# Optimization experiments

Measured on AMD Instinct MI355X. Metric: run time of the kernel, lower is better.

The kernel has to match this reference:

```python
import jax, jax.numpy as jnp
import numpy as np

B, S, HID = 2, 2048, 4096
NH, NKV, D = 32, 8, 128
GROUPS = NH // NKV


def _rotate_half(x):
    x1, x2 = jnp.split(x, 2, axis=-1)
    return jnp.concatenate((-x2, x1), axis=-1)


def setup_inputs() -> dict:
    key = jax.random.key(0)
    ks = jax.random.split(key, 5)
    hidden_states = jax.random.normal(ks[0], (B, S, HID), jnp.float32)
    Wq = jax.random.normal(ks[1], (HID, NH * D), jnp.float32) * (1.0 / np.float32(np.sqrt(HID)))
    Wk = jax.random.normal(ks[2], (HID, NKV * D), jnp.float32) * (1.0 / np.float32(np.sqrt(HID)))
    Wv = jax.random.normal(ks[3], (HID, NKV * D), jnp.float32) * (1.0 / np.float32(np.sqrt(HID)))
    Wo = jax.random.normal(ks[4], (NH * D, HID), jnp.float32) * (1.0 / np.float32(np.sqrt(NH * D)))
    # RoPE caches (Llama-style, base 10000)
    inv_freq = (1.0 / (10000.0 ** (np.arange(0, D, 2, dtype=np.float32) / D))).astype(np.float32)
    t = np.arange(S, dtype=np.float32)
    freqs = np.outer(t, inv_freq)  # [S, D/2]
    emb = np.concatenate([freqs, freqs], axis=-1)  # [S, D]
    cos_cache = jnp.asarray(np.cos(emb), jnp.float32)
    sin_cache = jnp.asarray(np.sin(emb), jnp.float32)
    position_ids = jnp.broadcast_to(jnp.arange(S, dtype=jnp.int64), (B, S))
    # causal mask used by scaled_qk's torch.where (True = attend)
    causal = jnp.tril(jnp.ones((S, S), dtype=bool))
    attention_mask = jnp.broadcast_to(causal[None, None], (B, 1, S, S))
    return {
        "hidden_states": hidden_states, "Wq": Wq, "Wk": Wk, "Wv": Wv, "Wo": Wo,
        "cos_cache": cos_cache, "sin_cache": sin_cache,
        "position_ids": position_ids, "attention_mask": attention_mask,
    }


def reference(hidden_states, Wq, Wk, Wv, Wo, cos_cache, sin_cache, position_ids, attention_mask):
    b, s, _ = hidden_states.shape
    # qkv_proj + move_heads_front -> [b, heads, s, d]
    Q = (hidden_states @ Wq).reshape(b, s, NH, D).transpose(0, 2, 1, 3)
    K = (hidden_states @ Wk).reshape(b, s, NKV, D).transpose(0, 2, 1, 3)
    V = (hidden_states @ Wv).reshape(b, s, NKV, D).transpose(0, 2, 1, 3)
    # RoPE
    cos = cos_cache[position_ids][:, None]  # [b,1,s,d]
    sin = sin_cache[position_ids][:, None]
    Q = Q * cos + _rotate_half(Q) * sin
    K = K * cos + _rotate_half(K) * sin
    # repeat_kv
    K = jnp.repeat(K, GROUPS, axis=1)  # [b,NH,s,d]
    V = jnp.repeat(V, GROUPS, axis=1)
    # scaled QK + mask + softmax (fp32) + PV
    scores = jnp.einsum("bhsd,bhtd->bhst", Q, K) / np.float32(np.sqrt(D))
    scores = jnp.where(attention_mask, scores, jnp.finfo(scores.dtype).min)
    probs = jax.nn.softmax(scores.astype(jnp.float32), axis=-1).astype(Q.dtype)
    attn = jnp.einsum("bhst,bhtd->bhsd", probs, V)
    # o_proj
    out = attn.transpose(0, 2, 1, 3).reshape(b, s, NH * D) @ Wo
    return out
```

## Files before the change

### kernel.cpp

```cpp
#include <hip/hip_runtime.h>

#define B_ 2
#define S_ 2048
#define HID_ 4096
#define NH_ 32
#define NKV_ 8
#define D_ 128
#define M_ (B_*S_)
#define NQKV_ (HID_ + 2*NKV_*D_)

typedef __bf16 v8bf __attribute__((ext_vector_type(8)));
typedef float  v4f  __attribute__((ext_vector_type(4)));

__device__ __forceinline__ unsigned short f2bf(float x) {
    unsigned u = __float_as_uint(x);
    u += 0x7FFFu + ((u >> 16) & 1u);
    return (unsigned short)(u >> 16);
}
__device__ __forceinline__ float bf2f(unsigned short h) {
    return __uint_as_float(((unsigned)h) << 16);
}

__device__ __forceinline__ void gl_lds16(const unsigned short* g, unsigned short* l) {
    __builtin_amdgcn_global_load_lds(
        (const __attribute__((address_space(1))) void*)g,
        (__attribute__((address_space(3))) void*)l, 16, 0, 0);
}

__global__ __launch_bounds__(256)
void cvt_f32_bf16(const float* __restrict__ src, unsigned short* __restrict__ dst, int n4) {
    int i = blockIdx.x * 256 + threadIdx.x;
    if (i >= n4) return;
    float4 v = ((const float4*)src)[i];
    ushort4 o;
    o.x = f2bf(v.x); o.y = f2bf(v.y); o.z = f2bf(v.z); o.w = f2bf(v.w);
    ((ushort4*)dst)[i] = o;
}

__global__ __launch_bounds__(256)
void transpose_f32_bf16(const float* __restrict__ src,
                        unsigned short* __restrict__ dst, int K, int N) {
    __shared__ unsigned short tile[64][65];
    int n0 = blockIdx.x * 64, k0 = blockIdx.y * 64;
    int tid = threadIdx.x;
    for (int i = 0; i < 16; ++i) {
        int fi = tid + i * 256;
        int r = fi >> 6, c = fi & 63;
        tile[r][c] = f2bf(src[(size_t)(k0 + r) * N + n0 + c]);
    }
    __syncthreads();
    for (int i = 0; i < 16; ++i) {
        int fi = tid + i * 256;
        int r = fi >> 6, c = fi & 63;
        dst[(size_t)(n0 + r) * K + k0 + c] = tile[c][r];
    }
}

__global__ __launch_bounds__(256)
void transpose_v(const unsigned short* __restrict__ src,
                 unsigned short* __restrict__ dst) {
    __shared__ unsigned short tile[64][65];
    int s0 = blockIdx.x * 64, d0 = blockIdx.y * 64;
    size_t base = (size_t)blockIdx.z * S_ * D_;
    int tid = threadIdx.x;
    for (int i = 0; i < 16; ++i) {
        int fi = tid + i * 256;
        int r = fi >> 6, c = fi & 63;
        tile[r][c] = src[base + (size_t)(s0 + r) * D_ + d0 + c];
    }
    __syncthreads();
    for (int i = 0; i < 16; ++i) {
        int fi = tid + i * 256;
        int r = fi >> 6, c = fi & 63;
        dst[base + (size_t)(d0 + r) * S_ + s0 + c] = tile[c][r];
    }
}

template <int MODE>
__global__ __launch_bounds__(256)
void gemm_bt(const unsigned short* __restrict__ A,
             const unsigned short* __restrict__ BT,
             int K, int lda, int ldb,
             unsigned short* __restrict__ outQ,
             unsigned short* __restrict__ outK,
             unsigned short* __restrict__ outV,
             float* __restrict__ outF) {
    __shared__ unsigned short As[128][32];
    __shared__ unsigned short Bs[128][32];
    int tid = threadIdx.x;
    int lane = tid & 63, wid = tid >> 6;
    int quad = lane >> 4, l16 = lane & 15;
    int wr = wid >> 1, wc = wid & 1;
    int r0 = blockIdx.y * 128, n0 = blockIdx.x * 128;

    v4f zero = {0.f, 0.f, 0.f, 0.f};
    v4f acc[4][4];
    for (int i = 0; i < 4; ++i) for (int j = 0; j < 4; ++j) acc[i][j] = zero;

    const int srow = wid * 32 + (lane >> 2);
    const int sch  = (lane & 3) * 8;
    const unsigned short* gA = &A [(size_t)(r0 + srow) * lda + sch];
    const unsigned short* gB = &BT[(size_t)(n0 + srow) * ldb + sch];
    unsigned short* lA0 = &As[wid * 32][0];
    unsigned short* lA1 = &As[wid * 32 + 16][0];
    unsigned short* lB0 = &Bs[wid * 32][0];
    unsigned short* lB1 = &Bs[wid * 32 + 16][0];

    for (int kt = 0; kt < K / 32; ++kt) {
        int kk = kt * 32;
        gl_lds16(gA + kk, lA0);
        gl_lds16(gA + (size_t)16 * lda + kk, lA1);
        gl_lds16(gB + kk, lB0);
        gl_lds16(gB + (size_t)16 * ldb + kk, lB1);
        __syncthreads();
        v8bf av[4], bv[4];
        for (int ms = 0; ms < 4; ++ms) av[ms] = *(const v8bf*)&As[wr * 64 + ms * 16 + l16][quad * 8];
        for (int ns = 0; ns < 4; ++ns) bv[ns] = *(const v8bf*)&Bs[wc * 64 + ns * 16 + l16][quad * 8];
        for (int ms = 0; ms < 4; ++ms)
            for (int ns = 0; ns < 4; ++ns)
                acc[ms][ns] = __builtin_amdgcn_mfma_f32_16x16x32_bf16(av[ms], bv[ns], acc[ms][ns], 0, 0, 0);
        __syncthreads();
    }

    for (int ms = 0; ms < 4; ++ms)
        for (int ns = 0; ns < 4; ++ns)
            for (int r = 0; r < 4; ++r) {
                int row = r0 + wr * 64 + ms * 16 + quad * 4 + r;
                int col = n0 + wc * 64 + ns * 16 + l16;
                if (MODE == 1) {
                    outF[(size_t)row * HID_ + col] = acc[ms][ns][r];
                } else {
                    unsigned short hv = f2bf(acc[ms][ns][r]);
                    int b = row >> 11, s = row & (S_ - 1);
                    if (col < HID_) {
                        int h = col >> 7, d = col & 127;
                        outQ[((size_t)((b * NH_ + h) * S_ + s)) * D_ + d] = hv;
                    } else if (col < HID_ + NKV_ * D_) {
                        int j = col - HID_; int h = j >> 7, d = j & 127;
                        outK[((size_t)((b * NKV_ + h) * S_ + s)) * D_ + d] = hv;
                    } else {
                        int j = col - HID_ - NKV_ * D_; int h = j >> 7, d = j & 127;
                        outV[((size_t)((b * NKV_ + h) * S_ + s)) * D_ + d] = hv;
                    }
                }
            }
}

__global__ __launch_bounds__(256)
void rope_kernel(unsigned short* __restrict__ buf,
                 const float* __restrict__ cosc,
                 const float* __restrict__ sinc, int total) {
    int idx = blockIdx.x * 256 + threadIdx.x;
    if (idx >= total) return;
    int d2 = idx & 63;
    int s  = (idx >> 6) & (S_ - 1);
    int bh = idx >> 17;
    size_t base = ((size_t)bh * S_ + s) * D_;
    float c  = cosc[s * D_ + d2];
    float sn = sinc[s * D_ + d2];
    float x1 = bf2f(buf[base + d2]);
    float x2 = bf2f(buf[base + d2 + 64]);
    buf[base + d2]      = f2bf(x1 * c - x2 * sn);
    buf[base + d2 + 64] = f2bf(x2 * c + x1 * sn);
}

__global__ __launch_bounds__(256)
void flash_attn(const unsigned short* __restrict__ Q,
                const unsigned short* __restrict__ Kb,
                const unsigned short* __restrict__ VT,
                unsigned short* __restrict__ O) {
    __shared__ unsigned short Ks[64][136];
    __shared__ unsigned short Vt[128][72];
    __shared__ unsigned short Ps[4][16][72];
    int tid = threadIdx.x;
    int lane = tid & 63, w = tid >> 6;
    int quad = lane >> 4, l16 = lane & 15;
    int qt = blockIdx.x, h = blockIdx.y, b = blockIdx.z;
    int qbase = qt * 64 + w * 16;

    const size_t qoff = ((size_t)(b * NH_ + h) * S_ + qbase + l16) * D_;
    v8bf aq[4];
    for (int kt = 0; kt < 4; ++kt) aq[kt] = *(const v8bf*)&Q[qoff + kt * 32 + quad * 8];

    const int hkv = h >> 2;
    const size_t kvbase = (size_t)(b * NKV_ + hkv) * S_ * D_;
    const size_t vtbase = kvbase;

    int krow[4], kch[4], vrow[4], vch[4];
    for (int i = 0; i < 4; ++i) {
        int idx = tid + i * 256;
        krow[i] = idx >> 4; kch[i] = idx & 15;
        vrow[i] = idx >> 3; vch[i] = idx & 7;
    }

    v4f zero = {0.f, 0.f, 0.f, 0.f};
    v4f o[8];
    for (int i = 0; i < 8; ++i) o[i] = zero;
    float m_[4] = {-1e30f, -1e30f, -1e30f, -1e30f};
    float l_[4] = {0.f, 0.f, 0.f, 0.f};

    const int ntiles = qt + 1;
    uint4 kpre[4], vpre[4];
    for (int i = 0; i < 4; ++i) {
        kpre[i] = *(const uint4*)&Kb[kvbase + (size_t)krow[i] * D_ + kch[i] * 8];
        vpre[i] = *(const uint4*)&VT[vtbase + (size_t)vrow[i] * S_ + vch[i] * 8];
    }

    for (int t = 0; t < ntiles; ++t) {
        int kv0 = t * 64;
        __syncthreads();
        for (int i = 0; i < 4; ++i) {
            *(uint4*)&Ks[krow[i]][kch[i] * 8] = kpre[i];
            *(uint4*)&Vt[vrow[i]][vch[i] * 8] = vpre[i];
        }
        __syncthreads();
        if (t + 1 < ntiles) {
            int nkv0 = kv0 + 64;
            for (int i = 0; i < 4; ++i) {
                kpre[i] = *(const uint4*)&Kb[kvbase + (size_t)(nkv0 + krow[i]) * D_ + kch[i] * 8];
                vpre[i] = *(const uint4*)&VT[vtbase + (size_t)vrow[i] * S_ + nkv0 + vch[i] * 8];
            }
        }

        v4f sa[4];
        for (int kg = 0; kg < 4; ++kg) sa[kg] = zero;
        for (int kg = 0; kg < 4; ++kg)
            for (int kt = 0; kt < 4; ++kt) {
                v8bf bk = *(const v8bf*)&Ks[kg * 16 + l16][kt * 32 + quad * 8];
                sa[kg] = __builtin_amdgcn_mfma_f32_16x16x32_bf16(aq[kt], bk, sa[kg], 0, 0, 0);
            }

        const float scale = 0.08838834764831845f;
        const bool diag = (t == qt);
        float p[4][4], al[4];
        for (int r = 0; r < 4; ++r) {
            int qrow = qbase + quad * 4 + r;
            float s0 = sa[0][r] * scale, s1 = sa[1][r] * scale;
            float s2 = sa[2][r] * scale, s3 = sa[3][r] * scale;
            if (diag) {
                if (kv0      + l16 > qrow) s0 = -1e30f;
                if (kv0 + 16 + l16 > qrow) s1 = -1e30f;
                if (kv0 + 32 + l16 > qrow) s2 = -1e30f;
                if (kv0 + 48 + l16 > qrow) s3 = -1e30f;
            }
            float rm = fmaxf(fmaxf(s0, s1), fmaxf(s2, s3));
            rm = fmaxf(rm, __shfl_xor(rm, 1));
            rm = fmaxf(rm, __shfl_xor(rm, 2));
            rm = fmaxf(rm, __shfl_xor(rm, 4));
            rm = fmaxf(rm, __shfl_xor(rm, 8));
            float mn = fmaxf(m_[r], rm);
            al[r] = __expf(m_[r] - mn);
            float p0 = __expf(s0 - mn), p1 = __expf(s1 - mn);
            float p2 = __expf(s2 - mn), p3 = __expf(s3 - mn);
            p[0][r] = p0; p[1][r] = p1; p[2][r] = p2; p[3][r] = p3;
            float rs = (p0 + p1) + (p2 + p3);
            rs += __shfl_xor(rs, 1);
            rs += __shfl_xor(rs, 2);
            rs += __shfl_xor(rs, 4);
            rs += __shfl_xor(rs, 8);
            l_[r] = l_[r] * al[r] + rs;
            m_[r] = mn;
        }
        for (int i = 0; i < 8; ++i)
            for (int r = 0; r < 4; ++r) o[i][r] *= al[r];

        for (int kg = 0; kg < 4; ++kg)
            for (int r = 0; r < 4; ++r)
                Ps[w][quad * 4 + r][kg * 16 + l16] = f2bf(p[kg][r]);
        v8bf pa0 = *(const v8bf*)&Ps[w][l16][quad * 8];
        v8bf pa1 = *(const v8bf*)&Ps[w][l16][32 + quad * 8];
        for (int n8 = 0; n8 < 8; ++n8) {
            v8bf bv0 = *(const v8bf*)&Vt[n8 * 16 + l16][quad * 8];
            v8bf bv1 = *(const v8bf*)&Vt[n8 * 16 + l16][32 + quad * 8];
            o[n8] = __builtin_amdgcn_mfma_f32_16x16x32_bf16(pa0, bv0, o[n8], 0, 0, 0);
            o[n8] = __builtin_amdgcn_mfma_f32_16x16x32_bf16(pa1, bv1, o[n8], 0, 0, 0);
        }
    }

    for (int n8 = 0; n8 < 8; ++n8)
        for (int r = 0; r < 4; ++r) {
            int qg = qbase + quad * 4 + r;
            float val = o[n8][r] / l_[r];
            O[((size_t)(b * S_ + qg)) * HID_ + h * D_ + n8 * 16 + l16] = f2bf(val);
        }
}

extern "C" void kernel_launch(void* const* d_in, const int* in_sizes, int n_in,
                              void* d_out, int out_size, void* d_ws, size_t ws_size,
                              hipStream_t stream) {
    const float* hid  = (const float*)d_in[0];
    const float* Wq   = (const float*)d_in[1];
    const float* Wk   = (const float*)d_in[2];
    const float* Wv   = (const float*)d_in[3];
    const float* Wo   = (const float*)d_in[4];
    const float* cosc = (const float*)d_in[5];
    const float* sinc = (const float*)d_in[6];

    unsigned short* ws    = (unsigned short*)d_ws;
    unsigned short* wqkvT = ws;
    unsigned short* qbuf  = ws + (size_t)NQKV_ * HID_;
    unsigned short* kbuf  = qbuf + (size_t)B_ * NH_ * S_ * D_;
    unsigned short* vbuf  = kbuf + (size_t)B_ * NKV_ * S_ * D_;
    unsigned short* hidB  = vbuf + (size_t)B_ * NKV_ * S_ * D_;
    unsigned short* attn  = ws;
    unsigned short* woT   = ws + (size_t)M_ * HID_;
    unsigned short* vTbuf = hidB;

    cvt_f32_bf16<<<(M_ * HID_ / 4 + 255) / 256, 256, 0, stream>>>(hid, hidB, M_ * HID_ / 4);
    transpose_f32_bf16<<<dim3(64, 64), 256, 0, stream>>>(Wq, wqkvT, HID_, HID_);
    transpose_f32_bf16<<<dim3(16, 64), 256, 0, stream>>>(Wk, wqkvT + (size_t)HID_ * HID_, HID_, NKV_ * D_);
    transpose_f32_bf16<<<dim3(16, 64), 256, 0, stream>>>(Wv, wqkvT + (size_t)(HID_ + NKV_ * D_) * HID_, HID_, NKV_ * D_);
    gemm_bt<0><<<dim3(NQKV_ / 128, M_ / 128), 256, 0, stream>>>(
        hidB, wqkvT, HID_, HID_, HID_, qbuf, kbuf, vbuf, nullptr);
    rope_kernel<<<(B_ * NH_ * S_ * 64) / 256, 256, 0, stream>>>(qbuf, cosc, sinc, B_ * NH_ * S_ * 64);
    rope_kernel<<<(B_ * NKV_ * S_ * 64) / 256, 256, 0, stream>>>(kbuf, cosc, sinc, B_ * NKV_ * S_ * 64);
    transpose_v<<<dim3(S_ / 64, D_ / 64, B_ * NKV_), 256, 0, stream>>>(vbuf, vTbuf);
    flash_attn<<<dim3(S_ / 64, NH_, B_), 256, 0, stream>>>(qbuf, kbuf, vTbuf, attn);
    transpose_f32_bf16<<<dim3(64, 64), 256, 0, stream>>>(Wo, woT, HID_, HID_);
    gemm_bt<1><<<dim3(HID_ / 128, M_ / 128), 256, 0, stream>>>(
        attn, woT, HID_, HID_, HID_, nullptr, nullptr, nullptr, (float*)d_out);
}
```

Measured before the change: 1.318 ms.

## Rewrite flash attention with 32x32 MFMA, 128-row Q tiles and register-resident P

The flash attention kernel moves from 16x16x32 to 32x32x16 bf16 MFMA and computes S transposed, so each lane owns one query row; row max and sum then need only a single cross-half shuffle. P stays in registers and is exchanged through lane shuffles instead of an LDS round trip. Q tiles grow to 128 rows per block and are scheduled longest-first, K in LDS gets an XOR swizzle to avoid bank conflicts, and softmax uses exp2 with a folded scale. The larger Q tile raises register pressure and may lower occupancy, and waves whose rows are already finished idle on barriers during the last K tiles.

```diff
diff --git a/kernel.cpp b/kernel.cpp
--- a/kernel.cpp
+++ b/kernel.cpp
@@ -11,6 +11,7 @@
 
 typedef __bf16 v8bf __attribute__((ext_vector_type(8)));
 typedef float  v4f  __attribute__((ext_vector_type(4)));
+typedef float  v16f __attribute__((ext_vector_type(16)));
 
 __device__ __forceinline__ unsigned short f2bf(float x) {
     unsigned u = __float_as_uint(x);
@@ -19,6 +20,12 @@
 }
 __device__ __forceinline__ float bf2f(unsigned short h) {
     return __uint_as_float(((unsigned)h) << 16);
+}
+__device__ __forceinline__ unsigned pack2bf(float a, float b) {
+    return (unsigned)f2bf(a) | ((unsigned)f2bf(b) << 16);
+}
+__device__ __forceinline__ float exp2g(float x) {
+    return __builtin_amdgcn_exp2f(x);
 }
 
 __device__ __forceinline__ void gl_lds16(const unsigned short* g, unsigned short* l) {
@@ -169,119 +176,154 @@
                 const unsigned short* __restrict__ Kb,
                 const unsigned short* __restrict__ VT,
                 unsigned short* __restrict__ O) {
-    __shared__ unsigned short Ks[64][136];
+    __shared__ unsigned short Ks[64 * 128];
     __shared__ unsigned short Vt[128][72];
-    __shared__ unsigned short Ps[4][16][72];
     int tid = threadIdx.x;
     int lane = tid & 63, w = tid >> 6;
-    int quad = lane >> 4, l16 = lane & 15;
-    int qt = blockIdx.x, h = blockIdx.y, b = blockIdx.z;
-    int qbase = qt * 64 + w * 16;
-
-    const size_t qoff = ((size_t)(b * NH_ + h) * S_ + qbase + l16) * D_;
-    v8bf aq[4];
-    for (int kt = 0; kt < 4; ++kt) aq[kt] = *(const v8bf*)&Q[qoff + kt * 32 + quad * 8];
+    int l31 = lane & 31, hi = lane >> 5;
+    int qt = 15 - (int)blockIdx.x;
+    int h = blockIdx.y, b = blockIdx.z;
+    int qbase = qt * 128 + w * 32;
+
+    const size_t qoff = ((size_t)(b * NH_ + h) * S_ + qbase + l31) * D_ + hi * 8;
+    v8bf aq[8];
+    #pragma unroll
+    for (int kt = 0; kt < 8; ++kt) aq[kt] = *(const v8bf*)&Q[qoff + kt * 16];
 
     const int hkv = h >> 2;
     const size_t kvbase = (size_t)(b * NKV_ + hkv) * S_ * D_;
     const size_t vtbase = kvbase;
 
     int krow[4], kch[4], vrow[4], vch[4];
+    #pragma unroll
     for (int i = 0; i < 4; ++i) {
         int idx = tid + i * 256;
         krow[i] = idx >> 4; kch[i] = idx & 15;
         vrow[i] = idx >> 3; vch[i] = idx & 7;
     }
 
-    v4f zero = {0.f, 0.f, 0.f, 0.f};
-    v4f o[8];
-    for (int i = 0; i < 8; ++i) o[i] = zero;
-    float m_[4] = {-1e30f, -1e30f, -1e30f, -1e30f};
-    float l_[4] = {0.f, 0.f, 0.f, 0.f};
-
-    const int ntiles = qt + 1;
+    v16f o[4];
+    #pragma unroll
+    for (int n = 0; n < 4; ++n)
+        #pragma unroll
+        for (int r = 0; r < 16; ++r) o[n][r] = 0.f;
+    float m2 = -1e30f, l_ = 0.f;
+
+    const int ntB = 2 * qt + 2;
+    const int twmax = (qbase + 31) >> 6;
+
     uint4 kpre[4], vpre[4];
+    #pragma unroll
     for (int i = 0; i < 4; ++i) {
         kpre[i] = *(const uint4*)&Kb[kvbase + (size_t)krow[i] * D_ + kch[i] * 8];
         vpre[i] = *(const uint4*)&VT[vtbase + (size_t)vrow[i] * S_ + vch[i] * 8];
     }
 
-    for (int t = 0; t < ntiles; ++t) {
+    for (int t = 0; t < ntB; ++t) {
         int kv0 = t * 64;
         __syncthreads();
+        #pragma unroll
         for (int i = 0; i < 4; ++i) {
-            *(uint4*)&Ks[krow[i]][kch[i] * 8] = kpre[i];
+            *(uint4*)&Ks[(size_t)krow[i] * 128 + ((kch[i] * 8) ^ ((krow[i] & 7) << 3))] = kpre[i];
             *(uint4*)&Vt[vrow[i]][vch[i] * 8] = vpre[i];
         }
         __syncthreads();
-        if (t + 1 < ntiles) {
+        if (t + 1 < ntB) {
             int nkv0 = kv0 + 64;
+            #pragma unroll
             for (int i = 0; i < 4; ++i) {
                 kpre[i] = *(const uint4*)&Kb[kvbase + (size_t)(nkv0 + krow[i]) * D_ + kch[i] * 8];
                 vpre[i] = *(const uint4*)&VT[vtbase + (size_t)vrow[i] * S_ + nkv0 + vch[i] * 8];
             }
         }
-
-        v4f sa[4];
-        for (int kg = 0; kg < 4; ++kg) sa[kg] = zero;
-        for (int kg = 0; kg < 4; ++kg)
-            for (int kt = 0; kt < 4; ++kt) {
-                v8bf bk = *(const v8bf*)&Ks[kg * 16 + l16][kt * 32 + quad * 8];
-                sa[kg] = __builtin_amdgcn_mfma_f32_16x16x32_bf16(aq[kt], bk, sa[kg], 0, 0, 0);
+        if (t > twmax) continue;
+
+        v16f s0, s1;
+        #pragma unroll
+        for (int r = 0; r < 16; ++r) { s0[r] = 0.f; s1[r] = 0.f; }
+        #pragma unroll
+        for (int kt = 0; kt < 8; ++kt) {
+            int cw = (kt * 16 + hi * 8) ^ ((l31 & 7) << 3);
+            v8bf k0 = *(const v8bf*)&Ks[(size_t)l31 * 128 + cw];
+            v8bf k1 = *(const v8bf*)&Ks[(size_t)(32 + l31) * 128 + cw];
+            s0 = __builtin_amdgcn_mfma_f32_32x32x16_bf16(k0, aq[kt], s0, 0, 0, 0);
+            s1 = __builtin_amdgcn_mfma_f32_32x32x16_bf16(k1, aq[kt], s1, 0, 0, 0);
+        }
+
+        if (kv0 + 63 > qbase) {
+            int vq = qbase + l31 - kv0 - 4 * hi;
+            #pragma unroll
+            for (int r = 0; r < 16; ++r) {
+                int c0 = (r & 3) + 8 * (r >> 2);
+                if (c0 > vq)      s0[r] = -1e30f;
+                if (c0 + 32 > vq) s1[r] = -1e30f;
             }
-
-        const float scale = 0.08838834764831845f;
-        const bool diag = (t == qt);
-        float p[4][4], al[4];
-        for (int r = 0; r < 4; ++r) {
-            int qrow = qbase + quad * 4 + r;
-            float s0 = sa[0][r] * scale, s1 = sa[1][r] * scale;
-            float s2 = sa[2][r] * scale, s3 = sa[3][r] * scale;
-            if (diag) {
-                if (kv0      + l16 > qrow) s0 = -1e30f;
-                if (kv0 + 16 + l16 > qrow) s1 = -1e30f;
-                if (kv0 + 32 + l16 > qrow) s2 = -1e30f;
-                if (kv0 + 48 + l16 > qrow) s3 = -1e30f;
+        }
+        float rm = fmaxf(s0[0], s1[0]);
+        #pragma unroll
+        for (int r = 1; r < 16; ++r) rm = fmaxf(rm, fmaxf(s0[r], s1[r]));
+        rm = fmaxf(rm, __shfl_xor(rm, 32));
+        const float cexp = 0.1275279431f;
+        float m2n = fmaxf(m2, rm * cexp);
+        float al = exp2g(m2 - m2n);
+        float rs = 0.f;
+        #pragma unroll
+        for (int r = 0; r < 16; ++r) {
+            s0[r] = exp2g(__builtin_fmaf(s0[r], cexp, -m2n));
+            s1[r] = exp2g(__builtin_fmaf(s1[r], cexp, -m2n));
+            rs += s0[r] + s1[r];
+        }
+        rs += __shfl_xor(rs, 32);
+        l_ = l_ * al + rs;
+        m2 = m2n;
+        #pragma unroll
+        for (int n = 0; n < 4; ++n)
+            #pragma unroll
+            for (int r = 0; r < 16; ++r) o[n][r] *= al;
+
+        unsigned pk0[4][2], pk1[4][2];
+        #pragma unroll
+        for (int g = 0; g < 4; ++g) {
+            pk0[g][0] = pack2bf(s0[4*g],   s0[4*g+1]);
+            pk0[g][1] = pack2bf(s0[4*g+2], s0[4*g+3]);
+            pk1[g][0] = pack2bf(s1[4*g],   s1[4*g+1]);
+            pk1[g][1] = pack2bf(s1[4*g+2], s1[4*g+3]);
+        }
+        const bool hb = (hi != 0);
+        #pragma unroll
+        for (int kb = 0; kb < 4; ++kb) {
+            const int g0 = (kb & 1) * 2;
+            unsigned la, lb, oa, ob;
+            if (kb < 2) { la = pk0[g0][0]; lb = pk0[g0][1]; oa = pk0[g0+1][0]; ob = pk0[g0+1][1]; }
+            else        { la = pk1[g0][0]; lb = pk1[g0][1]; oa = pk1[g0+1][0]; ob = pk1[g0+1][1]; }
+            unsigned sa0 = hb ? la : oa, sa1 = hb ? lb : ob;
+            unsigned ra0 = (unsigned)__shfl_xor((int)sa0, 32);
+            unsigned ra1 = (unsigned)__shfl_xor((int)sa1, 32);
+            unsigned ma0 = hb ? oa : la, ma1 = hb ? ob : lb;
+            union { unsigned u[4]; v8bf v; } pf;
+            pf.u[0] = hb ? ra0 : ma0; pf.u[1] = hb ? ra1 : ma1;
+            pf.u[2] = hb ? ma0 : ra0; pf.u[3] = hb ? ma1 : ra1;
+            #pragma unroll
+            for (int n = 0; n < 4; ++n) {
+                v8bf av = *(const v8bf*)&Vt[n * 32 + l31][kb * 16 + hi * 8];
+                o[n] = __builtin_amdgcn_mfma_f32_32x32x16_bf16(av, pf.v, o[n], 0, 0, 0);
             }
-            float rm = fmaxf(fmaxf(s0, s1), fmaxf(s2, s3));
-            rm = fmaxf(rm, __shfl_xor(rm, 1));
-            rm = fmaxf(rm, __shfl_xor(rm, 2));
-            rm = fmaxf(rm, __shfl_xor(rm, 4));
-            rm = fmaxf(rm, __shfl_xor(rm, 8));
-            float mn = fmaxf(m_[r], rm);
-            al[r] = __expf(m_[r] - mn);
-            float p0 = __expf(s0 - mn), p1 = __expf(s1 - mn);
-            float p2 = __expf(s2 - mn), p3 = __expf(s3 - mn);
-            p[0][r] = p0; p[1][r] = p1; p[2][r] = p2; p[3][r] = p3;
-            float rs = (p0 + p1) + (p2 + p3);
-            rs += __shfl_xor(rs, 1);
-            rs += __shfl_xor(rs, 2);
-            rs += __shfl_xor(rs, 4);
-            rs += __shfl_xor(rs, 8);
-            l_[r] = l_[r] * al[r] + rs;
-            m_[r] = mn;
-        }
-        for (int i = 0; i < 8; ++i)
-            for (int r = 0; r < 4; ++r) o[i][r] *= al[r];
-
-        for (int kg = 0; kg < 4; ++kg)
-            for (int r = 0; r < 4; ++r)
-                Ps[w][quad * 4 + r][kg * 16 + l16] = f2bf(p[kg][r]);
-        v8bf pa0 = *(const v8bf*)&Ps[w][l16][quad * 8];
-        v8bf pa1 = *(const v8bf*)&Ps[w][l16][32 + quad * 8];
-        for (int n8 = 0; n8 < 8; ++n8) {
-            v8bf bv0 = *(const v8bf*)&Vt[n8 * 16 + l16][quad * 8];
-            v8bf bv1 = *(const v8bf*)&Vt[n8 * 16 + l16][32 + quad * 8];
-            o[n8] = __builtin_amdgcn_mfma_f32_16x16x32_bf16(pa0, bv0, o[n8], 0, 0, 0);
-            o[n8] = __builtin_amdgcn_mfma_f32_16x16x32_bf16(pa1, bv1, o[n8], 0, 0, 0);
-        }
-    }
-
-    for (int n8 = 0; n8 < 8; ++n8)
-        for (int r = 0; r < 4; ++r) {
-            int qg = qbase + quad * 4 + r;
-            float val = o[n8][r] / l_[r];
-            O[((size_t)(b * S_ + qg)) * HID_ + h * D_ + n8 * 16 + l16] = f2bf(val);
+        }
+    }
+
+    float inv = 1.0f / l_;
+    int q = qbase + l31;
+    size_t obase = ((size_t)(b * S_ + q)) * HID_ + h * D_;
+    #pragma unroll
+    for (int n = 0; n < 4; ++n)
+        #pragma unroll
+        for (int rg = 0; rg < 4; ++rg) {
+            ushort4 st;
+            st.x = f2bf(o[n][4*rg+0] * inv);
+            st.y = f2bf(o[n][4*rg+1] * inv);
+            st.z = f2bf(o[n][4*rg+2] * inv);
+            st.w = f2bf(o[n][4*rg+3] * inv);
+            *(ushort4*)&O[obase + n * 32 + 8 * rg + 4 * hi] = st;
         }
 }
 
@@ -315,7 +357,7 @@
     rope_kernel<<<(B_ * NH_ * S_ * 64) / 256, 256, 0, stream>>>(qbuf, cosc, sinc, B_ * NH_ * S_ * 64);
     rope_kernel<<<(B_ * NKV_ * S_ * 64) / 256, 256, 0, stream>>>(kbuf, cosc, sinc, B_ * NKV_ * S_ * 64);
     transpose_v<<<dim3(S_ / 64, D_ / 64, B_ * NKV_), 256, 0, stream>>>(vbuf, vTbuf);
-    flash_attn<<<dim3(S_ / 64, NH_, B_), 256, 0, stream>>>(qbuf, kbuf, vTbuf, attn);
+    flash_attn<<<dim3(16, NH_, B_), 256, 0, stream>>>(qbuf, kbuf, vTbuf, attn);
     transpose_f32_bf16<<<dim3(64, 64), 256, 0, stream>>>(Wo, woT, HID_, HID_);
     gemm_bt<1><<<dim3(HID_ / 128, M_ / 128), 256, 0, stream>>>(
         attn, woT, HID_, HID_, HID_, nullptr, nullptr, nullptr, (float*)d_out);
```

New measurement: 1.185 ms. -10.1%, faster.
